# Performance work log

Measured on AMD Instinct MI355X. Metric: run time of the kernel, lower is better.

The kernel has to match this reference:

```python
import jax, jax.numpy as jnp
import numpy as np
import jax.ops

N_NODES = 50000
N_EDGES = 800000
N_GRAPHS = 512
F_IN = 128
HID = 256
N_CLASSES = 1

def _xavier(key, shape):
    fan_in, fan_out = shape[0], shape[1]
    std = (2.0 / (fan_in + fan_out)) ** 0.5
    return jax.random.normal(key, shape, dtype=jnp.float32) * std

def setup_inputs() -> dict:
    key = jax.random.key(0)
    ks = jax.random.split(key, 12)
    x = jax.random.normal(ks[0], (N_NODES, F_IN), dtype=jnp.float32)
    edge_index = jax.random.randint(ks[1], (2, N_EDGES), 0, N_NODES, dtype=jnp.int64)
    batch = jnp.sort(jax.random.randint(ks[2], (N_NODES,), 0, N_GRAPHS, dtype=jnp.int64))
    return {
        'x': x, 'edge_index': edge_index, 'batch': batch,
        'W0': _xavier(ks[3], (F_IN, HID)), 'b0': jnp.zeros((HID,), jnp.float32),
        'W1': _xavier(ks[4], (HID, HID)), 'b1': jnp.zeros((HID,), jnp.float32),
        'W2': _xavier(ks[5], (HID, HID)), 'b2': jnp.zeros((HID,), jnp.float32),
        'Wm1': _xavier(ks[6], (HID, HID)), 'bm1': jnp.zeros((HID,), jnp.float32),
        'Wm2': _xavier(ks[7], (HID, N_CLASSES)), 'bm2': jnp.zeros((N_CLASSES,), jnp.float32),
    }

def _gcn_layer(h, W, b, src, dst, deg_inv_sqrt):
    # PyG GCNConv: linear -> symmetric-normalized aggregation (with self loops) -> bias
    hw = h @ W                                        # [N, out]
    norm = deg_inv_sqrt[src] * deg_inv_sqrt[dst]      # [E]
    msg = hw[src] * norm[:, None]                     # [E, out]
    agg = jax.ops.segment_sum(msg, dst, num_segments=N_NODES)
    agg = agg + hw * (deg_inv_sqrt ** 2)[:, None]     # self-loop term
    return agg + b

def reference(x, edge_index, batch, W0, b0, W1, b1, W2, b2, Wm1, bm1, Wm2, bm2):
    src, dst = edge_index[0], edge_index[1]
    # degree with added self loops (in-degree at dst)
    deg = jax.ops.segment_sum(jnp.ones((N_EDGES,), jnp.float32), dst, num_segments=N_NODES) + 1.0
    deg_inv_sqrt = jax.lax.rsqrt(deg)
    h = jax.nn.relu(_gcn_layer(x, W0, b0, src, dst, deg_inv_sqrt))
    h = jax.nn.relu(_gcn_layer(h, W1, b1, src, dst, deg_inv_sqrt))
    h = jax.nn.relu(_gcn_layer(h, W2, b2, src, dst, deg_inv_sqrt))
    # global mean pool over graphs
    sums = jax.ops.segment_sum(h, batch, num_segments=N_GRAPHS)
    cnts = jax.ops.segment_sum(jnp.ones((N_NODES,), jnp.float32), batch, num_segments=N_GRAPHS)
    pooled = sums / jnp.maximum(cnts, 1.0)[:, None]   # [G, HID]
    out = jax.nn.relu(pooled @ Wm1 + bm1) @ Wm2 + bm2 # [G, num_classes]
    return out
```

## Files before the change

### kernel.cpp

```cpp
#include <hip/hip_runtime.h>

constexpr int N_NODES  = 50000;
constexpr int N_EDGES  = 800000;
constexpr int N_GRAPHS = 512;
constexpr int F_IN     = 128;
constexpr int HID      = 256;
constexpr int NPAD     = 50048;

typedef short short8 __attribute__((ext_vector_type(8)));
typedef float f32x4  __attribute__((ext_vector_type(4)));

__device__ __forceinline__ unsigned short f2b(float f) {
    unsigned u = __float_as_uint(f);
    u += 0x7fffu + ((u >> 16) & 1u);
    return (unsigned short)(u >> 16);
}
__device__ __forceinline__ float b2f_lo(unsigned u) { return __uint_as_float(u << 16); }
__device__ __forceinline__ float b2f_hi(unsigned u) { return __uint_as_float(u & 0xffff0000u); }

__global__ __launch_bounds__(256) void prep_kernel(
    const int* __restrict__ dst, int* __restrict__ deg,
    const float* __restrict__ x, unsigned short* __restrict__ x_bf,
    const float* __restrict__ W0, const float* __restrict__ W1, const float* __restrict__ W2,
    unsigned short* __restrict__ Wt0, unsigned short* __restrict__ Wt1, unsigned short* __restrict__ Wt2)
{
    const int b = blockIdx.x, t = threadIdx.x;
    if (b < 3125) {
        int e = b * 256 + t;
        atomicAdd(&deg[dst[e]], 1);
    } else if (b < 9375) {
        int i = (b - 3125) * 256 + t;
        float4 v = *reinterpret_cast<const float4*>(x + (size_t)i * 4);
        unsigned r0 = (unsigned)f2b(v.x) | ((unsigned)f2b(v.y) << 16);
        unsigned r1 = (unsigned)f2b(v.z) | ((unsigned)f2b(v.w) << 16);
        *reinterpret_cast<uint2*>(x_bf + (size_t)i * 4) = make_uint2(r0, r1);
    } else {
        int i = (b - 9375) * 256 + t;
        if (i < 32768)        { int k = i >> 8, n = i & 255;               Wt0[n * 128 + k] = f2b(W0[i]); }
        else if (i < 98304)   { int j = i - 32768; int k = j >> 8, n = j & 255; Wt1[n * 256 + k] = f2b(W1[j]); }
        else                  { int j = i - 98304; int k = j >> 8, n = j & 255; Wt2[n * 256 + k] = f2b(W2[j]); }
    }
}

__global__ void block_sum_dis_kernel(const int* __restrict__ deg, int* __restrict__ bsum,
                                     float* __restrict__ dis, int n) {
    __shared__ int sm[256];
    int t = threadIdx.x, base = blockIdx.x * 1024;
    int s = 0;
    #pragma unroll
    for (int i = 0; i < 4; ++i) {
        int idx = base + t + i * 256;
        if (idx < n) { int d = deg[idx]; s += d; dis[idx] = rsqrtf((float)d + 1.0f); }
    }
    sm[t] = s; __syncthreads();
    for (int o = 128; o > 0; o >>= 1) { if (t < o) sm[t] += sm[t + o]; __syncthreads(); }
    if (t == 0) bsum[blockIdx.x] = sm[0];
}

__global__ void scan_bsum_kernel(int* __restrict__ bsum, int nb) {
    __shared__ int sm[64];
    int t = threadIdx.x;
    int v = (t < nb) ? bsum[t] : 0;
    sm[t] = v; __syncthreads();
    for (int o = 1; o < 64; o <<= 1) {
        int a = (t >= o) ? sm[t - o] : 0; __syncthreads();
        sm[t] += a; __syncthreads();
    }
    if (t < nb) bsum[t] = sm[t] - v;
}

__global__ void scan_local_kernel(const int* __restrict__ deg, const int* __restrict__ bsum,
                                  int* __restrict__ row_start, int* __restrict__ cursor, int n) {
    __shared__ int sm[256];
    int t = threadIdx.x, base = blockIdx.x * 1024;
    int idx0 = base + t * 4;
    int v[4], s = 0;
    #pragma unroll
    for (int i = 0; i < 4; ++i) { int id = idx0 + i; v[i] = (id < n) ? deg[id] : 0; s += v[i]; }
    sm[t] = s; __syncthreads();
    for (int o = 1; o < 256; o <<= 1) {
        int a = (t >= o) ? sm[t - o] : 0; __syncthreads();
        sm[t] += a; __syncthreads();
    }
    int excl = bsum[blockIdx.x] + sm[t] - s;
    #pragma unroll
    for (int i = 0; i < 4; ++i) {
        int id = idx0 + i;
        if (id < n) { row_start[id] = excl; cursor[id] = excl; }
        excl += v[i];
    }
    if (blockIdx.x == gridDim.x - 1 && t == 255) row_start[n] = excl;
}

__global__ void fill_csr(const int* __restrict__ src, const int* __restrict__ dst,
                         const float* __restrict__ dis, int* __restrict__ cursor,
                         int2* __restrict__ csr) {
    int e = blockIdx.x * blockDim.x + threadIdx.x;
    if (e >= N_EDGES) return;
    int s = src[e], d = dst[e];
    int pos = atomicAdd(&cursor[d], 1);
    float w = dis[s] * dis[d];
    csr[pos] = make_int2(s, __float_as_int(w));
}

template<int F>
__global__ __launch_bounds__(256) void agg_bf16(
    const unsigned short* __restrict__ hin, const int* __restrict__ row_start,
    const int2* __restrict__ csr, const float* __restrict__ dis,
    unsigned short* __restrict__ out)
{
    constexpr int LPR  = F / 8;
    constexpr int NSUB = 64 / LPR;
    const int lane = threadIdx.x & 63;
    const int sub  = lane / LPR;
    const int fc   = lane % LPR;
    const int node = blockIdx.x * 4 + (threadIdx.x >> 6);
    if (node >= N_NODES) return;

    float acc[8];
    {
        float dn = dis[node];
        float sw = (sub == 0) ? dn * dn : 0.0f;
        uint2 u2[2];
        *reinterpret_cast<uint4*>(u2) =
            *reinterpret_cast<const uint4*>(hin + (size_t)node * F + fc * 8);
        #pragma unroll
        for (int h = 0; h < 2; ++h) {
            acc[h * 4 + 0] = b2f_lo(u2[h].x) * sw;
            acc[h * 4 + 1] = b2f_hi(u2[h].x) * sw;
            acc[h * 4 + 2] = b2f_lo(u2[h].y) * sw;
            acc[h * 4 + 3] = b2f_hi(u2[h].y) * sw;
        }
    }

    int j = row_start[node] + sub;
    const int end = row_start[node + 1];
    for (; j + 3 * NSUB < end; j += 4 * NSUB) {
        int2 c[4];
        #pragma unroll
        for (int u = 0; u < 4; ++u) c[u] = csr[j + u * NSUB];
        #pragma unroll
        for (int u = 0; u < 4; ++u) {
            float w = __int_as_float(c[u].y);
            uint2 g[2];
            *reinterpret_cast<uint4*>(g) =
                *reinterpret_cast<const uint4*>(hin + (size_t)c[u].x * F + fc * 8);
            #pragma unroll
            for (int h = 0; h < 2; ++h) {
                acc[h * 4 + 0] = fmaf(b2f_lo(g[h].x), w, acc[h * 4 + 0]);
                acc[h * 4 + 1] = fmaf(b2f_hi(g[h].x), w, acc[h * 4 + 1]);
                acc[h * 4 + 2] = fmaf(b2f_lo(g[h].y), w, acc[h * 4 + 2]);
                acc[h * 4 + 3] = fmaf(b2f_hi(g[h].y), w, acc[h * 4 + 3]);
            }
        }
    }
    for (; j < end; j += NSUB) {
        int2 c0 = csr[j];
        float w = __int_as_float(c0.y);
        uint2 g[2];
        *reinterpret_cast<uint4*>(g) =
            *reinterpret_cast<const uint4*>(hin + (size_t)c0.x * F + fc * 8);
        #pragma unroll
        for (int h = 0; h < 2; ++h) {
            acc[h * 4 + 0] = fmaf(b2f_lo(g[h].x), w, acc[h * 4 + 0]);
            acc[h * 4 + 1] = fmaf(b2f_hi(g[h].x), w, acc[h * 4 + 1]);
            acc[h * 4 + 2] = fmaf(b2f_lo(g[h].y), w, acc[h * 4 + 2]);
            acc[h * 4 + 3] = fmaf(b2f_hi(g[h].y), w, acc[h * 4 + 3]);
        }
    }

    #pragma unroll
    for (int k = 0; k < 8; ++k) {
        #pragma unroll
        for (int off = LPR; off < 64; off <<= 1)
            acc[k] += __shfl_xor(acc[k], off, 64);
    }

    if (sub == 0) {
        uint2 r[2];
        #pragma unroll
        for (int h = 0; h < 2; ++h) {
            r[h].x = (unsigned)f2b(acc[h * 4 + 0]) | ((unsigned)f2b(acc[h * 4 + 1]) << 16);
            r[h].y = (unsigned)f2b(acc[h * 4 + 2]) | ((unsigned)f2b(acc[h * 4 + 3]) << 16);
        }
        *reinterpret_cast<uint4*>(out + (size_t)node * F + fc * 8) =
            *reinterpret_cast<uint4*>(r);
    }
}

template<int K>
__global__ __launch_bounds__(256) void gemm_mfma(
    const unsigned short* __restrict__ A,
    const unsigned short* __restrict__ Bt,
    const float* __restrict__ bias,
    unsigned short* __restrict__ C,
    int relu)
{
    __shared__ __align__(16) unsigned short As[2][4 * 128 * 8];
    __shared__ __align__(16) unsigned short Bs[2][4 * 128 * 8];
    const int t    = threadIdx.x;
    const int lane = t & 63;
    const int w    = t >> 6;
    const int wm   = w & 1, wn = w >> 1;
    const int q    = lane >> 4, m = lane & 15;
    const int row0 = blockIdx.x * 128;
    const int col0 = blockIdx.y * 128;
    const int r_   = t >> 2, c_ = t & 3;

    f32x4 acc[4][4] = {};

    auto stage = [&](int buf, int k0) {
        #pragma unroll
        for (int pass = 0; pass < 2; ++pass) {
            int r = r_ + pass * 64;
            uint4 av = *reinterpret_cast<const uint4*>(A  + (size_t)(row0 + r) * K + k0 + c_ * 8);
            uint4 bv = *reinterpret_cast<const uint4*>(Bt + (size_t)(col0 + r) * K + k0 + c_ * 8);
            *reinterpret_cast<uint4*>(&As[buf][(c_ * 128 + r) * 8]) = av;
            *reinterpret_cast<uint4*>(&Bs[buf][(c_ * 128 + r) * 8]) = bv;
        }
    };

    constexpr int NK = K / 32;
    stage(0, 0);
    __syncthreads();
    #pragma unroll
    for (int kb = 0; kb < NK; ++kb) {
        if (kb + 1 < NK) stage((kb + 1) & 1, (kb + 1) * 32);
        const unsigned short* as = As[kb & 1];
        const unsigned short* bs = Bs[kb & 1];
        short8 af[4], bf[4];
        #pragma unroll
        for (int i = 0; i < 4; ++i)
            af[i] = *reinterpret_cast<const short8*>(&as[(q * 128 + wm * 64 + i * 16 + m) * 8]);
        #pragma unroll
        for (int jn = 0; jn < 4; ++jn)
            bf[jn] = *reinterpret_cast<const short8*>(&bs[(q * 128 + wn * 64 + jn * 16 + m) * 8]);
        #pragma unroll
        for (int i = 0; i < 4; ++i)
            #pragma unroll
            for (int jn = 0; jn < 4; ++jn)
                acc[i][jn] = __builtin_amdgcn_mfma_f32_16x16x32_bf16(af[i], bf[jn], acc[i][jn], 0, 0, 0);
        __syncthreads();
    }

    #pragma unroll
    for (int jn = 0; jn < 4; ++jn) {
        int col = col0 + wn * 64 + jn * 16 + m;
        float bj = bias[col];
        #pragma unroll
        for (int i = 0; i < 4; ++i) {
            int rowb = row0 + wm * 64 + i * 16 + q * 4;
            #pragma unroll
            for (int r = 0; r < 4; ++r) {
                float v = acc[i][jn][r] + bj;
                if (relu) v = fmaxf(v, 0.f);
                C[(size_t)(rowb + r) * 256 + col] = f2b(v);
            }
        }
    }
}

__global__ __launch_bounds__(256) void pool_mlp_kernel(
    const unsigned short* __restrict__ h, const int* __restrict__ batch,
    const float* __restrict__ Wm1, const float* __restrict__ bm1,
    const float* __restrict__ Wm2, const float* __restrict__ bm2,
    float* __restrict__ out)
{
    __shared__ float p[HID];
    __shared__ float red[HID];
    __shared__ int se[2];
    const int g = blockIdx.x, t = threadIdx.x;
    if (t < 2) {
        int target = g + t;
        int lo = 0, hi = N_NODES;
        while (lo < hi) { int mid = (lo + hi) >> 1; if (batch[mid] < target) lo = mid + 1; else hi = mid; }
        se[t] = lo;
    }
    __syncthreads();
    const int s = se[0], e = se[1];
    float acc = 0.f;
    for (int n = s; n < e; ++n) acc += b2f_lo((unsigned)h[(size_t)n * HID + t]);
    p[t] = acc / fmaxf((float)(e - s), 1.0f);
    __syncthreads();
    float a2 = bm1[t];
    for (int k = 0; k < HID; ++k) a2 = fmaf(p[k], Wm1[k * HID + t], a2);
    red[t] = fmaxf(a2, 0.f) * Wm2[t];
    __syncthreads();
    for (int o = 128; o > 0; o >>= 1) {
        if (t < o) red[t] += red[t + o];
        __syncthreads();
    }
    if (t == 0) out[g] = red[0] + bm2[0];
}

extern "C" void kernel_launch(void* const* d_in, const int* in_sizes, int n_in,
                              void* d_out, int out_size, void* d_ws, size_t ws_size,
                              hipStream_t stream) {
    const float* x    = (const float*)d_in[0];
    const int*   ei   = (const int*)d_in[1];
    const int*   batch= (const int*)d_in[2];
    const float* W0   = (const float*)d_in[3];
    const float* b0   = (const float*)d_in[4];
    const float* W1   = (const float*)d_in[5];
    const float* b1   = (const float*)d_in[6];
    const float* W2   = (const float*)d_in[7];
    const float* b2   = (const float*)d_in[8];
    const float* Wm1  = (const float*)d_in[9];
    const float* bm1  = (const float*)d_in[10];
    const float* Wm2  = (const float*)d_in[11];
    const float* bm2  = (const float*)d_in[12];
    float* out = (float*)d_out;

    char* ws = (char*)d_ws;
    size_t off = 0;
    auto alloc = [&](size_t bytes) -> void* {
        void* p = ws + off;
        off += (bytes + 255) & ~(size_t)255;
        return p;
    };
    int*   deg       = (int*)  alloc((size_t)N_NODES * 4);
    float* dis       = (float*)alloc((size_t)N_NODES * 4);
    int*   row_start = (int*)  alloc((size_t)(N_NODES + 1) * 4);
    int*   cursor    = (int*)  alloc((size_t)N_NODES * 4);
    int*   bsum      = (int*)  alloc((size_t)64 * 4);
    int2*  csr       = (int2*) alloc((size_t)N_EDGES * 8);
    unsigned short* x_bf = (unsigned short*)alloc((size_t)N_NODES * F_IN * 2);
    unsigned short* Wt0  = (unsigned short*)alloc((size_t)F_IN * HID * 2);
    unsigned short* Wt1  = (unsigned short*)alloc((size_t)HID * HID * 2);
    unsigned short* Wt2  = (unsigned short*)alloc((size_t)HID * HID * 2);
    unsigned short* bufA = (unsigned short*)alloc((size_t)NPAD * HID * 2);
    unsigned short* bufB = (unsigned short*)alloc((size_t)NPAD * HID * 2);

    const int* src = ei;
    const int* dst = ei + N_EDGES;
    const int NB = (N_NODES + 1023) / 1024;

    hipMemsetAsync(deg, 0, (size_t)N_NODES * 4, stream);
    prep_kernel        <<<10015, 256, 0, stream>>>(dst, deg, x, x_bf, W0, W1, W2, Wt0, Wt1, Wt2);
    block_sum_dis_kernel<<<NB, 256, 0, stream>>>(deg, bsum, dis, N_NODES);
    scan_bsum_kernel   <<<1, 64, 0, stream>>>(bsum, NB);
    scan_local_kernel  <<<NB, 256, 0, stream>>>(deg, bsum, row_start, cursor, N_NODES);
    fill_csr           <<<(N_EDGES + 255) / 256, 256, 0, stream>>>(src, dst, dis, cursor, csr);

    dim3 ggrid(NPAD / 128, 2);

    agg_bf16<F_IN><<<(N_NODES + 3) / 4, 256, 0, stream>>>(x_bf, row_start, csr, dis, bufA);
    gemm_mfma<F_IN><<<ggrid, 256, 0, stream>>>(bufA, Wt0, b0, bufB, 1);

    agg_bf16<HID><<<(N_NODES + 3) / 4, 256, 0, stream>>>(bufB, row_start, csr, dis, bufA);
    gemm_mfma<HID><<<ggrid, 256, 0, stream>>>(bufA, Wt1, b1, bufB, 1);

    agg_bf16<HID><<<(N_NODES + 3) / 4, 256, 0, stream>>>(bufB, row_start, csr, dis, bufA);
    gemm_mfma<HID><<<ggrid, 256, 0, stream>>>(bufA, Wt2, b2, bufB, 1);

    pool_mlp_kernel<<<N_GRAPHS, HID, 0, stream>>>(bufB, batch, Wm1, bm1, Wm2, bm2, out);
}
```

Before: 435.8 us.

## Write aggregation output in MFMA fragment layout and load A directly in GEMM

The aggregation kernel now writes its bf16 output in a panel/k-chunk-major layout that matches the MFMA A-fragment order. The GEMM reads A fragments straight from global memory without going through LDS, and the weights are pre-swizzled into fragment order and staged whole into LDS once per block. This removes the per-k-step A/B staging, the double buffering and the barriers. In exchange, A loads are no longer software-prefetched, and the LDS footprint is larger (64 KB for K=256), which may limit occupancy.

After: 430.9 us. About the same (-1.1%).

```diff
diff --git a/kernel.cpp b/kernel.cpp
--- a/kernel.cpp
+++ b/kernel.cpp
@@ -36,9 +36,13 @@
         *reinterpret_cast<uint2*>(x_bf + (size_t)i * 4) = make_uint2(r0, r1);
     } else {
         int i = (b - 9375) * 256 + t;
-        if (i < 32768)        { int k = i >> 8, n = i & 255;               Wt0[n * 128 + k] = f2b(W0[i]); }
-        else if (i < 98304)   { int j = i - 32768; int k = j >> 8, n = j & 255; Wt1[n * 256 + k] = f2b(W1[j]); }
-        else                  { int j = i - 98304; int k = j >> 8, n = j & 255; Wt2[n * 256 + k] = f2b(W2[j]); }
+        const float* W; unsigned short* Wt; int K; int j;
+        if (i < 32768)      { W = W0; Wt = Wt0; K = 128; j = i; }
+        else if (i < 98304) { W = W1; Wt = Wt1; K = 256; j = i - 32768; }
+        else                { W = W2; Wt = Wt2; K = 256; j = i - 98304; }
+        int k = j >> 8, n = j & 255;
+        int idx = (n >> 7) * (K * 128) + (((k >> 3) * 128 + (n & 127)) << 3) + (k & 7);
+        Wt[idx] = f2b(W[j]);
     }
 }
 
@@ -107,7 +111,7 @@
 __global__ __launch_bounds__(256) void agg_bf16(
     const unsigned short* __restrict__ hin, const int* __restrict__ row_start,
     const int2* __restrict__ csr, const float* __restrict__ dis,
-    unsigned short* __restrict__ out)
+    uint4* __restrict__ out4)
 {
     constexpr int LPR  = F / 8;
     constexpr int NSUB = 64 / LPR;
@@ -183,64 +187,56 @@
             r[h].x = (unsigned)f2b(acc[h * 4 + 0]) | ((unsigned)f2b(acc[h * 4 + 1]) << 16);
             r[h].y = (unsigned)f2b(acc[h * 4 + 2]) | ((unsigned)f2b(acc[h * 4 + 3]) << 16);
         }
-        *reinterpret_cast<uint4*>(out + (size_t)node * F + fc * 8) =
-            *reinterpret_cast<uint4*>(r);
+        int chunk = (node >> 7) * (128 * (F / 8)) + fc * 128 + (node & 127);
+        out4[chunk] = *reinterpret_cast<uint4*>(r);
     }
 }
 
 template<int K>
-__global__ __launch_bounds__(256) void gemm_mfma(
-    const unsigned short* __restrict__ A,
-    const unsigned short* __restrict__ Bt,
+__global__ __launch_bounds__(256) void gemm_frag(
+    const uint4* __restrict__ A4,
+    const unsigned short* __restrict__ Wt_frag,
     const float* __restrict__ bias,
     unsigned short* __restrict__ C,
     int relu)
 {
-    __shared__ __align__(16) unsigned short As[2][4 * 128 * 8];
-    __shared__ __align__(16) unsigned short Bs[2][4 * 128 * 8];
+    __shared__ __align__(16) unsigned short Bs[K * 128];
     const int t    = threadIdx.x;
     const int lane = t & 63;
     const int w    = t >> 6;
     const int wm   = w & 1, wn = w >> 1;
     const int q    = lane >> 4, m = lane & 15;
-    const int row0 = blockIdx.x * 128;
-    const int col0 = blockIdx.y * 128;
-    const int r_   = t >> 2, c_ = t & 3;
+    const int panel = blockIdx.x;
+    const int col0  = blockIdx.y * 128;
+
+    {
+        const uint4* src4 = reinterpret_cast<const uint4*>(Wt_frag + blockIdx.y * (K * 128));
+        uint4* dst4 = reinterpret_cast<uint4*>(Bs);
+        #pragma unroll
+        for (int it = 0; it < K / 16; ++it)
+            dst4[it * 256 + t] = src4[it * 256 + t];
+    }
+    __syncthreads();
 
     f32x4 acc[4][4] = {};
-
-    auto stage = [&](int buf, int k0) {
-        #pragma unroll
-        for (int pass = 0; pass < 2; ++pass) {
-            int r = r_ + pass * 64;
-            uint4 av = *reinterpret_cast<const uint4*>(A  + (size_t)(row0 + r) * K + k0 + c_ * 8);
-            uint4 bv = *reinterpret_cast<const uint4*>(Bt + (size_t)(col0 + r) * K + k0 + c_ * 8);
-            *reinterpret_cast<uint4*>(&As[buf][(c_ * 128 + r) * 8]) = av;
-            *reinterpret_cast<uint4*>(&Bs[buf][(c_ * 128 + r) * 8]) = bv;
-        }
-    };
-
-    constexpr int NK = K / 32;
-    stage(0, 0);
-    __syncthreads();
-    #pragma unroll
-    for (int kb = 0; kb < NK; ++kb) {
-        if (kb + 1 < NK) stage((kb + 1) & 1, (kb + 1) * 32);
-        const unsigned short* as = As[kb & 1];
-        const unsigned short* bs = Bs[kb & 1];
+    const int abase = panel * (128 * (K / 8));
+
+    #pragma unroll
+    for (int kb = 0; kb < K / 32; ++kb) {
         short8 af[4], bf[4];
         #pragma unroll
-        for (int i = 0; i < 4; ++i)
-            af[i] = *reinterpret_cast<const short8*>(&as[(q * 128 + wm * 64 + i * 16 + m) * 8]);
+        for (int i = 0; i < 4; ++i) {
+            uint4 v = A4[abase + (kb * 4 + q) * 128 + wm * 64 + i * 16 + m];
+            af[i] = *reinterpret_cast<short8*>(&v);
+        }
         #pragma unroll
         for (int jn = 0; jn < 4; ++jn)
-            bf[jn] = *reinterpret_cast<const short8*>(&bs[(q * 128 + wn * 64 + jn * 16 + m) * 8]);
+            bf[jn] = *reinterpret_cast<const short8*>(&Bs[((kb * 4 + q) * 128 + wn * 64 + jn * 16 + m) * 8]);
         #pragma unroll
         for (int i = 0; i < 4; ++i)
             #pragma unroll
             for (int jn = 0; jn < 4; ++jn)
                 acc[i][jn] = __builtin_amdgcn_mfma_f32_16x16x32_bf16(af[i], bf[jn], acc[i][jn], 0, 0, 0);
-        __syncthreads();
     }
 
     #pragma unroll
@@ -249,7 +245,7 @@
         float bj = bias[col];
         #pragma unroll
         for (int i = 0; i < 4; ++i) {
-            int rowb = row0 + wm * 64 + i * 16 + q * 4;
+            int rowb = panel * 128 + wm * 64 + i * 16 + q * 4;
             #pragma unroll
             for (int r = 0; r < 4; ++r) {
                 float v = acc[i][jn][r] + bj;
@@ -336,22 +332,22 @@
     const int NB = (N_NODES + 1023) / 1024;
 
     hipMemsetAsync(deg, 0, (size_t)N_NODES * 4, stream);
-    prep_kernel        <<<10015, 256, 0, stream>>>(dst, deg, x, x_bf, W0, W1, W2, Wt0, Wt1, Wt2);
+    prep_kernel         <<<10015, 256, 0, stream>>>(dst, deg, x, x_bf, W0, W1, W2, Wt0, Wt1, Wt2);
     block_sum_dis_kernel<<<NB, 256, 0, stream>>>(deg, bsum, dis, N_NODES);
-    scan_bsum_kernel   <<<1, 64, 0, stream>>>(bsum, NB);
-    scan_local_kernel  <<<NB, 256, 0, stream>>>(deg, bsum, row_start, cursor, N_NODES);
-    fill_csr           <<<(N_EDGES + 255) / 256, 256, 0, stream>>>(src, dst, dis, cursor, csr);
+    scan_bsum_kernel    <<<1, 64, 0, stream>>>(bsum, NB);
+    scan_local_kernel   <<<NB, 256, 0, stream>>>(deg, bsum, row_start, cursor, N_NODES);
+    fill_csr            <<<(N_EDGES + 255) / 256, 256, 0, stream>>>(src, dst, dis, cursor, csr);
 
     dim3 ggrid(NPAD / 128, 2);
 
-    agg_bf16<F_IN><<<(N_NODES + 3) / 4, 256, 0, stream>>>(x_bf, row_start, csr, dis, bufA);
-    gemm_mfma<F_IN><<<ggrid, 256, 0, stream>>>(bufA, Wt0, b0, bufB, 1);
-
-    agg_bf16<HID><<<(N_NODES + 3) / 4, 256, 0, stream>>>(bufB, row_start, csr, dis, bufA);
-    gemm_mfma<HID><<<ggrid, 256, 0, stream>>>(bufA, Wt1, b1, bufB, 1);
-
-    agg_bf16<HID><<<(N_NODES + 3) / 4, 256, 0, stream>>>(bufB, row_start, csr, dis, bufA);
-    gemm_mfma<HID><<<ggrid, 256, 0, stream>>>(bufA, Wt2, b2, bufB, 1);
+    agg_bf16<F_IN><<<(N_NODES + 3) / 4, 256, 0, stream>>>(x_bf, row_start, csr, dis, (uint4*)bufA);
+    gemm_frag<F_IN><<<ggrid, 256, 0, stream>>>((const uint4*)bufA, Wt0, b0, bufB, 1);
+
+    agg_bf16<HID><<<(N_NODES + 3) / 4, 256, 0, stream>>>(bufB, row_start, csr, dis, (uint4*)bufA);
+    gemm_frag<HID><<<ggrid, 256, 0, stream>>>((const uint4*)bufA, Wt1, b1, bufB, 1);
+
+    agg_bf16<HID><<<(N_NODES + 3) / 4, 256, 0, stream>>>(bufB, row_start, csr, dis, (uint4*)bufA);
+    gemm_frag<HID><<<ggrid, 256, 0, stream>>>((const uint4*)bufA, Wt2, b2, bufB, 1);
 
     pool_mlp_kernel<<<N_GRAPHS, HID, 0, stream>>>(bufB, batch, Wm1, bm1, Wm2, bm2, out);
 }
```

## Slice aggregation by feature chunk per XCD and pack CSR entries to 32 bits

Applied to the files above, without the earlier changes.

Aggregation now splits the feature dimension into 64-column slices and maps each slice to a fixed XCD via blockIdx&7, so each XCD's L2 only caches one slice of the gathered feature matrix. Each block walks 64 nodes in a loop instead of one node per wavefront. CSR entries shrink from 8 bytes to 4 by packing a 16-bit source index with a bf16 edge weight, which halves index traffic but loses weight precision and relies on node ids fitting in 16 bits (50000 < 65536). Separate h1/h2 buffers are used so layers can ping-pong.

After: 499.8 us. +14.7%, slower.

```diff
diff --git a/kernel.cpp b/kernel.cpp
--- a/kernel.cpp
+++ b/kernel.cpp
@@ -36,9 +36,12 @@
         *reinterpret_cast<uint2*>(x_bf + (size_t)i * 4) = make_uint2(r0, r1);
     } else {
         int i = (b - 9375) * 256 + t;
-        if (i < 32768)        { int k = i >> 8, n = i & 255;               Wt0[n * 128 + k] = f2b(W0[i]); }
-        else if (i < 98304)   { int j = i - 32768; int k = j >> 8, n = j & 255; Wt1[n * 256 + k] = f2b(W1[j]); }
-        else                  { int j = i - 98304; int k = j >> 8, n = j & 255; Wt2[n * 256 + k] = f2b(W2[j]); }
+        const float* W; unsigned short* Wt; int K; int j;
+        if (i < 32768)      { W = W0; Wt = Wt0; K = 128; j = i; }
+        else if (i < 98304) { W = W1; Wt = Wt1; K = 256; j = i - 32768; }
+        else                { W = W2; Wt = Wt2; K = 256; j = i - 98304; }
+        int k = j >> 8, n = j & 255;
+        Wt[n * K + k] = f2b(W[j]);
     }
 }
 
@@ -94,97 +97,110 @@
 
 __global__ void fill_csr(const int* __restrict__ src, const int* __restrict__ dst,
                          const float* __restrict__ dis, int* __restrict__ cursor,
-                         int2* __restrict__ csr) {
+                         unsigned* __restrict__ csr) {
     int e = blockIdx.x * blockDim.x + threadIdx.x;
     if (e >= N_EDGES) return;
     int s = src[e], d = dst[e];
     int pos = atomicAdd(&cursor[d], 1);
     float w = dis[s] * dis[d];
-    csr[pos] = make_int2(s, __float_as_int(w));
-}
-
-template<int F>
-__global__ __launch_bounds__(256) void agg_bf16(
+    csr[pos] = ((unsigned)f2b(w) << 16) | (unsigned)s;
+}
+
+template<int K, int NSLICE, int CHG>
+__global__ __launch_bounds__(256) void agg_sliced(
     const unsigned short* __restrict__ hin, const int* __restrict__ row_start,
-    const int2* __restrict__ csr, const float* __restrict__ dis,
+    const unsigned* __restrict__ csr, const float* __restrict__ dis,
     unsigned short* __restrict__ out)
 {
-    constexpr int LPR  = F / 8;
-    constexpr int NSUB = 64 / LPR;
-    const int lane = threadIdx.x & 63;
-    const int sub  = lane / LPR;
-    const int fc   = lane % LPR;
-    const int node = blockIdx.x * 4 + (threadIdx.x >> 6);
-    if (node >= N_NODES) return;
-
-    float acc[8];
-    {
-        float dn = dis[node];
-        float sw = (sub == 0) ? dn * dn : 0.0f;
-        uint2 u2[2];
-        *reinterpret_cast<uint4*>(u2) =
-            *reinterpret_cast<const uint4*>(hin + (size_t)node * F + fc * 8);
-        #pragma unroll
-        for (int h = 0; h < 2; ++h) {
-            acc[h * 4 + 0] = b2f_lo(u2[h].x) * sw;
-            acc[h * 4 + 1] = b2f_hi(u2[h].x) * sw;
-            acc[h * 4 + 2] = b2f_lo(u2[h].y) * sw;
-            acc[h * 4 + 3] = b2f_hi(u2[h].y) * sw;
-        }
-    }
-
-    int j = row_start[node] + sub;
-    const int end = row_start[node + 1];
-    for (; j + 3 * NSUB < end; j += 4 * NSUB) {
-        int2 c[4];
-        #pragma unroll
-        for (int u = 0; u < 4; ++u) c[u] = csr[j + u * NSUB];
-        #pragma unroll
-        for (int u = 0; u < 4; ++u) {
-            float w = __int_as_float(c[u].y);
-            uint2 g[2];
-            *reinterpret_cast<uint4*>(g) =
-                *reinterpret_cast<const uint4*>(hin + (size_t)c[u].x * F + fc * 8);
-            #pragma unroll
-            for (int h = 0; h < 2; ++h) {
-                acc[h * 4 + 0] = fmaf(b2f_lo(g[h].x), w, acc[h * 4 + 0]);
-                acc[h * 4 + 1] = fmaf(b2f_hi(g[h].x), w, acc[h * 4 + 1]);
-                acc[h * 4 + 2] = fmaf(b2f_lo(g[h].y), w, acc[h * 4 + 2]);
-                acc[h * 4 + 3] = fmaf(b2f_hi(g[h].y), w, acc[h * 4 + 3]);
-            }
-        }
-    }
-    for (; j < end; j += NSUB) {
-        int2 c0 = csr[j];
-        float w = __int_as_float(c0.y);
-        uint2 g[2];
-        *reinterpret_cast<uint4*>(g) =
-            *reinterpret_cast<const uint4*>(hin + (size_t)c0.x * F + fc * 8);
-        #pragma unroll
-        for (int h = 0; h < 2; ++h) {
-            acc[h * 4 + 0] = fmaf(b2f_lo(g[h].x), w, acc[h * 4 + 0]);
-            acc[h * 4 + 1] = fmaf(b2f_hi(g[h].x), w, acc[h * 4 + 1]);
-            acc[h * 4 + 2] = fmaf(b2f_lo(g[h].y), w, acc[h * 4 + 2]);
-            acc[h * 4 + 3] = fmaf(b2f_hi(g[h].y), w, acc[h * 4 + 3]);
-        }
-    }
-
-    #pragma unroll
-    for (int k = 0; k < 8; ++k) {
-        #pragma unroll
-        for (int off = LPR; off < 64; off <<= 1)
-            acc[k] += __shfl_xor(acc[k], off, 64);
-    }
-
-    if (sub == 0) {
-        uint2 r[2];
-        #pragma unroll
-        for (int h = 0; h < 2; ++h) {
-            r[h].x = (unsigned)f2b(acc[h * 4 + 0]) | ((unsigned)f2b(acc[h * 4 + 1]) << 16);
-            r[h].y = (unsigned)f2b(acc[h * 4 + 2]) | ((unsigned)f2b(acc[h * 4 + 3]) << 16);
-        }
-        *reinterpret_cast<uint4*>(out + (size_t)node * F + fc * 8) =
-            *reinterpret_cast<uint4*>(r);
+    const int b     = blockIdx.x;
+    const int xcd   = b & 7;
+    const int gp    = b >> 3;
+    const int slice = xcd % NSLICE;
+    const int chunk = gp + (xcd / NSLICE) * CHG;
+    const int t     = threadIdx.x;
+    const int lane  = t & 63;
+    const int w     = t >> 6;
+    const int sub   = lane >> 3;
+    const int fc    = lane & 7;
+    const int foff  = slice * 64 + fc * 8;
+
+    for (int nn = 0; nn < 16; ++nn) {
+        const int node = chunk * 64 + w * 16 + nn;
+        if (node >= N_NODES) break;
+
+        float acc[8];
+        {
+            float dn = dis[node];
+            float sw = (sub == 0) ? dn * dn : 0.0f;
+            uint2 u2[2];
+            *reinterpret_cast<uint4*>(u2) =
+                *reinterpret_cast<const uint4*>(hin + (size_t)node * K + foff);
+            #pragma unroll
+            for (int h = 0; h < 2; ++h) {
+                acc[h * 4 + 0] = b2f_lo(u2[h].x) * sw;
+                acc[h * 4 + 1] = b2f_hi(u2[h].x) * sw;
+                acc[h * 4 + 2] = b2f_lo(u2[h].y) * sw;
+                acc[h * 4 + 3] = b2f_hi(u2[h].y) * sw;
+            }
+        }
+
+        int j = row_start[node] + sub;
+        const int end = row_start[node + 1];
+        for (; j + 8 < end; j += 16) {
+            unsigned c0 = csr[j], c1 = csr[j + 8];
+            float w0 = b2f_hi(c0), w1 = b2f_hi(c1);
+            uint2 g0[2], g1[2];
+            *reinterpret_cast<uint4*>(g0) =
+                *reinterpret_cast<const uint4*>(hin + (size_t)(c0 & 0xffffu) * K + foff);
+            *reinterpret_cast<uint4*>(g1) =
+                *reinterpret_cast<const uint4*>(hin + (size_t)(c1 & 0xffffu) * K + foff);
+            #pragma unroll
+            for (int h = 0; h < 2; ++h) {
+                acc[h * 4 + 0] = fmaf(b2f_lo(g0[h].x), w0, acc[h * 4 + 0]);
+                acc[h * 4 + 1] = fmaf(b2f_hi(g0[h].x), w0, acc[h * 4 + 1]);
+                acc[h * 4 + 2] = fmaf(b2f_lo(g0[h].y), w0, acc[h * 4 + 2]);
+                acc[h * 4 + 3] = fmaf(b2f_hi(g0[h].y), w0, acc[h * 4 + 3]);
+            }
+            #pragma unroll
+            for (int h = 0; h < 2; ++h) {
+                acc[h * 4 + 0] = fmaf(b2f_lo(g1[h].x), w1, acc[h * 4 + 0]);
+                acc[h * 4 + 1] = fmaf(b2f_hi(g1[h].x), w1, acc[h * 4 + 1]);
+                acc[h * 4 + 2] = fmaf(b2f_lo(g1[h].y), w1, acc[h * 4 + 2]);
+                acc[h * 4 + 3] = fmaf(b2f_hi(g1[h].y), w1, acc[h * 4 + 3]);
+            }
+        }
+        if (j < end) {
+            unsigned c0 = csr[j];
+            float w0 = b2f_hi(c0);
+            uint2 g0[2];
+            *reinterpret_cast<uint4*>(g0) =
+                *reinterpret_cast<const uint4*>(hin + (size_t)(c0 & 0xffffu) * K + foff);
+            #pragma unroll
+            for (int h = 0; h < 2; ++h) {
+                acc[h * 4 + 0] = fmaf(b2f_lo(g0[h].x), w0, acc[h * 4 + 0]);
+                acc[h * 4 + 1] = fmaf(b2f_hi(g0[h].x), w0, acc[h * 4 + 1]);
+                acc[h * 4 + 2] = fmaf(b2f_lo(g0[h].y), w0, acc[h * 4 + 2]);
+                acc[h * 4 + 3] = fmaf(b2f_hi(g0[h].y), w0, acc[h * 4 + 3]);
+            }
+        }
+
+        #pragma unroll
+        for (int k = 0; k < 8; ++k) {
+            #pragma unroll
+            for (int off = 8; off < 64; off <<= 1)
+                acc[k] += __shfl_xor(acc[k], off, 64);
+        }
+
+        if (sub == 0) {
+            uint2 rv[2];
+            #pragma unroll
+            for (int h = 0; h < 2; ++h) {
+                rv[h].x = (unsigned)f2b(acc[h * 4 + 0]) | ((unsigned)f2b(acc[h * 4 + 1]) << 16);
+                rv[h].y = (unsigned)f2b(acc[h * 4 + 2]) | ((unsigned)f2b(acc[h * 4 + 3]) << 16);
+            }
+            *reinterpret_cast<uint4*>(out + (size_t)node * K + foff) =
+                *reinterpret_cast<uint4*>(rv);
+        }
     }
 }
 
@@ -318,40 +334,41 @@
         off += (bytes + 255) & ~(size_t)255;
         return p;
     };
-    int*   deg       = (int*)  alloc((size_t)N_NODES * 4);
-    float* dis       = (float*)alloc((size_t)N_NODES * 4);
-    int*   row_start = (int*)  alloc((size_t)(N_NODES + 1) * 4);
-    int*   cursor    = (int*)  alloc((size_t)N_NODES * 4);
-    int*   bsum      = (int*)  alloc((size_t)64 * 4);
-    int2*  csr       = (int2*) alloc((size_t)N_EDGES * 8);
+    int*      deg       = (int*)     alloc((size_t)N_NODES * 4);
+    float*    dis       = (float*)   alloc((size_t)N_NODES * 4);
+    int*      row_start = (int*)     alloc((size_t)(N_NODES + 1) * 4);
+    int*      cursor    = (int*)     alloc((size_t)N_NODES * 4);
+    int*      bsum      = (int*)     alloc((size_t)64 * 4);
+    unsigned* csr       = (unsigned*)alloc((size_t)N_EDGES * 4);
     unsigned short* x_bf = (unsigned short*)alloc((size_t)N_NODES * F_IN * 2);
     unsigned short* Wt0  = (unsigned short*)alloc((size_t)F_IN * HID * 2);
     unsigned short* Wt1  = (unsigned short*)alloc((size_t)HID * HID * 2);
     unsigned short* Wt2  = (unsigned short*)alloc((size_t)HID * HID * 2);
     unsigned short* bufA = (unsigned short*)alloc((size_t)NPAD * HID * 2);
-    unsigned short* bufB = (unsigned short*)alloc((size_t)NPAD * HID * 2);
+    unsigned short* h1   = (unsigned short*)alloc((size_t)NPAD * HID * 2);
+    unsigned short* h2   = (unsigned short*)alloc((size_t)NPAD * HID * 2);
 
     const int* src = ei;
     const int* dst = ei + N_EDGES;
     const int NB = (N_NODES + 1023) / 1024;
 
     hipMemsetAsync(deg, 0, (size_t)N_NODES * 4, stream);
-    prep_kernel        <<<10015, 256, 0, stream>>>(dst, deg, x, x_bf, W0, W1, W2, Wt0, Wt1, Wt2);
+    prep_kernel         <<<10015, 256, 0, stream>>>(dst, deg, x, x_bf, W0, W1, W2, Wt0, Wt1, Wt2);
     block_sum_dis_kernel<<<NB, 256, 0, stream>>>(deg, bsum, dis, N_NODES);
-    scan_bsum_kernel   <<<1, 64, 0, stream>>>(bsum, NB);
-    scan_local_kernel  <<<NB, 256, 0, stream>>>(deg, bsum, row_start, cursor, N_NODES);
-    fill_csr           <<<(N_EDGES + 255) / 256, 256, 0, stream>>>(src, dst, dis, cursor, csr);
+    scan_bsum_kernel    <<<1, 64, 0, stream>>>(bsum, NB);
+    scan_local_kernel   <<<NB, 256, 0, stream>>>(deg, bsum, row_start, cursor, N_NODES);
+    fill_csr            <<<(N_EDGES + 255) / 256, 256, 0, stream>>>(src, dst, dis, cursor, csr);
 
     dim3 ggrid(NPAD / 128, 2);
 
-    agg_bf16<F_IN><<<(N_NODES + 3) / 4, 256, 0, stream>>>(x_bf, row_start, csr, dis, bufA);
-    gemm_mfma<F_IN><<<ggrid, 256, 0, stream>>>(bufA, Wt0, b0, bufB, 1);
-
-    agg_bf16<HID><<<(N_NODES + 3) / 4, 256, 0, stream>>>(bufB, row_start, csr, dis, bufA);
-    gemm_mfma<HID><<<ggrid, 256, 0, stream>>>(bufA, Wt1, b1, bufB, 1);
-
-    agg_bf16<HID><<<(N_NODES + 3) / 4, 256, 0, stream>>>(bufB, row_start, csr, dis, bufA);
-    gemm_mfma<HID><<<ggrid, 256, 0, stream>>>(bufA, Wt2, b2, bufB, 1);
-
-    pool_mlp_kernel<<<N_GRAPHS, HID, 0, stream>>>(bufB, batch, Wm1, bm1, Wm2, bm2, out);
-}
+    agg_sliced<128, 2, 196><<<1568, 256, 0, stream>>>(x_bf, row_start, csr, dis, bufA);
+    gemm_mfma<128><<<ggrid, 256, 0, stream>>>(bufA, Wt0, b0, h1, 1);
+
+    agg_sliced<256, 4, 391><<<3128, 256, 0, stream>>>(h1, row_start, csr, dis, bufA);
+    gemm_mfma<256><<<ggrid, 256, 0, stream>>>(bufA, Wt1, b1, h2, 1);
+
+    agg_sliced<256, 4, 391><<<3128, 256, 0, stream>>>(h2, row_start, csr, dis, bufA);
+    gemm_mfma<256><<<ggrid, 256, 0, stream>>>(bufA, Wt2, b2, h1, 1);
+
+    pool_mlp_kernel<<<N_GRAPHS, HID, 0, stream>>>(h1, batch, Wm1, bm1, Wm2, bm2, out);
+}
```

## Fuse graph preprocessing into one cooperative kernel and pack CSR entries

Applied to the files above, without the earlier changes.

Replaces the memset, prep, block-sum, scan and CSR-fill launches with one cooperative kernel. Its phases (degree counting, scan, CSR fill) are separated by grid-wide syncs. CSR entries shrink from 8 bytes to 4 by packing a 16-bit source index with a bf16 edge weight. This cuts launch overhead and CSR bandwidth in the three aggregation passes, at the cost of lower precision in the edge weights and a grid size fixed by cooperative-launch occupancy.

Result: slower. 685.9 us (+57.4%).

```diff
diff --git a/kernel.cpp b/kernel.cpp
--- a/kernel.cpp
+++ b/kernel.cpp
@@ -1,4 +1,7 @@
 #include <hip/hip_runtime.h>
+#include <hip/hip_cooperative_groups.h>
+
+namespace cg = cooperative_groups;
 
 constexpr int N_NODES  = 50000;
 constexpr int N_EDGES  = 800000;
@@ -6,6 +9,8 @@
 constexpr int F_IN     = 128;
 constexpr int HID      = 256;
 constexpr int NPAD     = 50048;
+constexpr int PBLK     = 512;
+constexpr int SPAN     = 98;
 
 typedef short short8 __attribute__((ext_vector_type(8)));
 typedef float f32x4  __attribute__((ext_vector_type(4)));
@@ -18,98 +23,94 @@
 __device__ __forceinline__ float b2f_lo(unsigned u) { return __uint_as_float(u << 16); }
 __device__ __forceinline__ float b2f_hi(unsigned u) { return __uint_as_float(u & 0xffff0000u); }
 
-__global__ __launch_bounds__(256) void prep_kernel(
-    const int* __restrict__ dst, int* __restrict__ deg,
-    const float* __restrict__ x, unsigned short* __restrict__ x_bf,
+__device__ __forceinline__ int lds_scan_incl(int* sm, int v) {
+    const int t = threadIdx.x;
+    sm[t] = v; __syncthreads();
+    #pragma unroll
+    for (int o = 1; o < 256; o <<= 1) {
+        int a = (t >= o) ? sm[t - o] : 0; __syncthreads();
+        sm[t] += a; __syncthreads();
+    }
+    return sm[t];
+}
+
+__global__ __launch_bounds__(256, 2) void prep_all(
+    const int* __restrict__ src, const int* __restrict__ dst,
+    const float* __restrict__ x,
     const float* __restrict__ W0, const float* __restrict__ W1, const float* __restrict__ W2,
-    unsigned short* __restrict__ Wt0, unsigned short* __restrict__ Wt1, unsigned short* __restrict__ Wt2)
+    int* deg, float* dis, int* row_start, int* cursor, int* bsum, unsigned* csr,
+    unsigned short* x_bf, unsigned short* Wt0, unsigned short* Wt1, unsigned short* Wt2)
 {
-    const int b = blockIdx.x, t = threadIdx.x;
-    if (b < 3125) {
-        int e = b * 256 + t;
-        atomicAdd(&deg[dst[e]], 1);
-    } else if (b < 9375) {
-        int i = (b - 3125) * 256 + t;
+    __shared__ int sm[256];
+    cg::grid_group grid = cg::this_grid();
+    const int t   = threadIdx.x;
+    const int b   = blockIdx.x;
+    const int gid = b * 256 + t;
+    const int gstride = PBLK * 256;
+
+    for (int i = gid; i < N_NODES; i += gstride) deg[i] = 0;
+    for (int i = gid; i < N_NODES * F_IN / 4; i += gstride) {
         float4 v = *reinterpret_cast<const float4*>(x + (size_t)i * 4);
         unsigned r0 = (unsigned)f2b(v.x) | ((unsigned)f2b(v.y) << 16);
         unsigned r1 = (unsigned)f2b(v.z) | ((unsigned)f2b(v.w) << 16);
         *reinterpret_cast<uint2*>(x_bf + (size_t)i * 4) = make_uint2(r0, r1);
-    } else {
-        int i = (b - 9375) * 256 + t;
-        if (i < 32768)        { int k = i >> 8, n = i & 255;               Wt0[n * 128 + k] = f2b(W0[i]); }
-        else if (i < 98304)   { int j = i - 32768; int k = j >> 8, n = j & 255; Wt1[n * 256 + k] = f2b(W1[j]); }
-        else                  { int j = i - 98304; int k = j >> 8, n = j & 255; Wt2[n * 256 + k] = f2b(W2[j]); }
-    }
-}
-
-__global__ void block_sum_dis_kernel(const int* __restrict__ deg, int* __restrict__ bsum,
-                                     float* __restrict__ dis, int n) {
-    __shared__ int sm[256];
-    int t = threadIdx.x, base = blockIdx.x * 1024;
-    int s = 0;
-    #pragma unroll
-    for (int i = 0; i < 4; ++i) {
-        int idx = base + t + i * 256;
-        if (idx < n) { int d = deg[idx]; s += d; dis[idx] = rsqrtf((float)d + 1.0f); }
-    }
-    sm[t] = s; __syncthreads();
-    for (int o = 128; o > 0; o >>= 1) { if (t < o) sm[t] += sm[t + o]; __syncthreads(); }
-    if (t == 0) bsum[blockIdx.x] = sm[0];
-}
-
-__global__ void scan_bsum_kernel(int* __restrict__ bsum, int nb) {
-    __shared__ int sm[64];
-    int t = threadIdx.x;
-    int v = (t < nb) ? bsum[t] : 0;
-    sm[t] = v; __syncthreads();
-    for (int o = 1; o < 64; o <<= 1) {
-        int a = (t >= o) ? sm[t - o] : 0; __syncthreads();
-        sm[t] += a; __syncthreads();
-    }
-    if (t < nb) bsum[t] = sm[t] - v;
-}
-
-__global__ void scan_local_kernel(const int* __restrict__ deg, const int* __restrict__ bsum,
-                                  int* __restrict__ row_start, int* __restrict__ cursor, int n) {
-    __shared__ int sm[256];
-    int t = threadIdx.x, base = blockIdx.x * 1024;
-    int idx0 = base + t * 4;
-    int v[4], s = 0;
-    #pragma unroll
-    for (int i = 0; i < 4; ++i) { int id = idx0 + i; v[i] = (id < n) ? deg[id] : 0; s += v[i]; }
-    sm[t] = s; __syncthreads();
-    for (int o = 1; o < 256; o <<= 1) {
-        int a = (t >= o) ? sm[t - o] : 0; __syncthreads();
-        sm[t] += a; __syncthreads();
-    }
-    int excl = bsum[blockIdx.x] + sm[t] - s;
-    #pragma unroll
-    for (int i = 0; i < 4; ++i) {
-        int id = idx0 + i;
-        if (id < n) { row_start[id] = excl; cursor[id] = excl; }
-        excl += v[i];
-    }
-    if (blockIdx.x == gridDim.x - 1 && t == 255) row_start[n] = excl;
-}
-
-__global__ void fill_csr(const int* __restrict__ src, const int* __restrict__ dst,
-                         const float* __restrict__ dis, int* __restrict__ cursor,
-                         int2* __restrict__ csr) {
-    int e = blockIdx.x * blockDim.x + threadIdx.x;
-    if (e >= N_EDGES) return;
-    int s = src[e], d = dst[e];
-    int pos = atomicAdd(&cursor[d], 1);
-    float w = dis[s] * dis[d];
-    csr[pos] = make_int2(s, __float_as_int(w));
-}
-
-template<int F>
+    }
+    for (int i = gid; i < 163840; i += gstride) {
+        const float* W; unsigned short* Wt; int K, j;
+        if (i < 32768)      { W = W0; Wt = Wt0; K = 128; j = i; }
+        else if (i < 98304) { W = W1; Wt = Wt1; K = 256; j = i - 32768; }
+        else                { W = W2; Wt = Wt2; K = 256; j = i - 98304; }
+        int k = j >> 8, n = j & 255;
+        Wt[n * K + k] = f2b(W[j]);
+    }
+    grid.sync();
+
+    for (int e = gid; e < N_EDGES; e += gstride) atomicAdd(&deg[dst[e]], 1);
+    grid.sync();
+
+    {
+        int node = b * SPAN + t;
+        int d = 0;
+        if (t < SPAN && node < N_NODES) { d = deg[node]; dis[node] = rsqrtf((float)d + 1.0f); }
+        sm[t] = d; __syncthreads();
+        #pragma unroll
+        for (int o = 128; o > 0; o >>= 1) { if (t < o) sm[t] += sm[t + o]; __syncthreads(); }
+        if (t == 0) bsum[b] = sm[0];
+    }
+    grid.sync();
+
+    {
+        int pv = bsum[2 * t] + bsum[2 * t + 1];
+        lds_scan_incl(sm, pv);
+        const int p = b >> 1;
+        int Pb = (p > 0) ? sm[p - 1] : 0;
+        if (b & 1) Pb += bsum[2 * p];
+        const int grand = sm[255];
+        __syncthreads();
+        int node = b * SPAN + t;
+        int v = (t < SPAN && node < N_NODES) ? deg[node] : 0;
+        int incl = lds_scan_incl(sm, v);
+        int excl = incl - v + Pb;
+        if (t < SPAN && node < N_NODES) { row_start[node] = excl; cursor[node] = excl; }
+        if (b == PBLK - 1 && t == 0) row_start[N_NODES] = grand;
+    }
+    grid.sync();
+
+    for (int e = gid; e < N_EDGES; e += gstride) {
+        int s = src[e], d = dst[e];
+        int pos = atomicAdd(&cursor[d], 1);
+        float w = dis[s] * dis[d];
+        csr[pos] = ((unsigned)f2b(w) << 16) | (unsigned)s;
+    }
+}
+
+template<int K>
 __global__ __launch_bounds__(256) void agg_bf16(
     const unsigned short* __restrict__ hin, const int* __restrict__ row_start,
-    const int2* __restrict__ csr, const float* __restrict__ dis,
+    const unsigned* __restrict__ csr, const float* __restrict__ dis,
     unsigned short* __restrict__ out)
 {
-    constexpr int LPR  = F / 8;
+    constexpr int LPR  = K / 8;
     constexpr int NSUB = 64 / LPR;
     const int lane = threadIdx.x & 63;
     const int sub  = lane / LPR;
@@ -123,7 +124,7 @@
         float sw = (sub == 0) ? dn * dn : 0.0f;
         uint2 u2[2];
         *reinterpret_cast<uint4*>(u2) =
-            *reinterpret_cast<const uint4*>(hin + (size_t)node * F + fc * 8);
+            *reinterpret_cast<const uint4*>(hin + (size_t)node * K + fc * 8);
         #pragma unroll
         for (int h = 0; h < 2; ++h) {
             acc[h * 4 + 0] = b2f_lo(u2[h].x) * sw;
@@ -136,15 +137,15 @@
     int j = row_start[node] + sub;
     const int end = row_start[node + 1];
     for (; j + 3 * NSUB < end; j += 4 * NSUB) {
-        int2 c[4];
+        unsigned c[4];
         #pragma unroll
         for (int u = 0; u < 4; ++u) c[u] = csr[j + u * NSUB];
         #pragma unroll
         for (int u = 0; u < 4; ++u) {
-            float w = __int_as_float(c[u].y);
+            float w = b2f_hi(c[u]);
             uint2 g[2];
             *reinterpret_cast<uint4*>(g) =
-                *reinterpret_cast<const uint4*>(hin + (size_t)c[u].x * F + fc * 8);
+                *reinterpret_cast<const uint4*>(hin + (size_t)(c[u] & 0xffffu) * K + fc * 8);
             #pragma unroll
             for (int h = 0; h < 2; ++h) {
                 acc[h * 4 + 0] = fmaf(b2f_lo(g[h].x), w, acc[h * 4 + 0]);
@@ -155,11 +156,11 @@
         }
     }
     for (; j < end; j += NSUB) {
-        int2 c0 = csr[j];
-        float w = __int_as_float(c0.y);
+        unsigned c0 = csr[j];
+        float w = b2f_hi(c0);
         uint2 g[2];
         *reinterpret_cast<uint4*>(g) =
-            *reinterpret_cast<const uint4*>(hin + (size_t)c0.x * F + fc * 8);
+            *reinterpret_cast<const uint4*>(hin + (size_t)(c0 & 0xffffu) * K + fc * 8);
         #pragma unroll
         for (int h = 0; h < 2; ++h) {
             acc[h * 4 + 0] = fmaf(b2f_lo(g[h].x), w, acc[h * 4 + 0]);
@@ -177,14 +178,14 @@
     }
 
     if (sub == 0) {
-        uint2 r[2];
+        uint2 rv[2];
         #pragma unroll
         for (int h = 0; h < 2; ++h) {
-            r[h].x = (unsigned)f2b(acc[h * 4 + 0]) | ((unsigned)f2b(acc[h * 4 + 1]) << 16);
-            r[h].y = (unsigned)f2b(acc[h * 4 + 2]) | ((unsigned)f2b(acc[h * 4 + 3]) << 16);
-        }
-        *reinterpret_cast<uint4*>(out + (size_t)node * F + fc * 8) =
-            *reinterpret_cast<uint4*>(r);
+            rv[h].x = (unsigned)f2b(acc[h * 4 + 0]) | ((unsigned)f2b(acc[h * 4 + 1]) << 16);
+            rv[h].y = (unsigned)f2b(acc[h * 4 + 2]) | ((unsigned)f2b(acc[h * 4 + 3]) << 16);
+        }
+        *reinterpret_cast<uint4*>(out + (size_t)node * K + fc * 8) =
+            *reinterpret_cast<uint4*>(rv);
     }
 }
 
@@ -318,40 +319,41 @@
         off += (bytes + 255) & ~(size_t)255;
         return p;
     };
-    int*   deg       = (int*)  alloc((size_t)N_NODES * 4);
-    float* dis       = (float*)alloc((size_t)N_NODES * 4);
-    int*   row_start = (int*)  alloc((size_t)(N_NODES + 1) * 4);
-    int*   cursor    = (int*)  alloc((size_t)N_NODES * 4);
-    int*   bsum      = (int*)  alloc((size_t)64 * 4);
-    int2*  csr       = (int2*) alloc((size_t)N_EDGES * 8);
+    int*      deg       = (int*)     alloc((size_t)N_NODES * 4);
+    float*    dis       = (float*)   alloc((size_t)N_NODES * 4);
+    int*      row_start = (int*)     alloc((size_t)(N_NODES + 1) * 4);
+    int*      cursor    = (int*)     alloc((size_t)N_NODES * 4);
+    int*      bsum      = (int*)     alloc((size_t)PBLK * 4);
+    unsigned* csr       = (unsigned*)alloc((size_t)N_EDGES * 4);
     unsigned short* x_bf = (unsigned short*)alloc((size_t)N_NODES * F_IN * 2);
     unsigned short* Wt0  = (unsigned short*)alloc((size_t)F_IN * HID * 2);
     unsigned short* Wt1  = (unsigned short*)alloc((size_t)HID * HID * 2);
     unsigned short* Wt2  = (unsigned short*)alloc((size_t)HID * HID * 2);
     unsigned short* bufA = (unsigned short*)alloc((size_t)NPAD * HID * 2);
-    unsigned short* bufB = (unsigned short*)alloc((size_t)NPAD * HID * 2);
-
-    const int* src = ei;
-    const int* dst = ei + N_EDGES;
-    const int NB = (N_NODES + 1023) / 1024;
-
-    hipMemsetAsync(deg, 0, (size_t)N_NODES * 4, stream);
-    prep_kernel        <<<10015, 256, 0, stream>>>(dst, deg, x, x_bf, W0, W1, W2, Wt0, Wt1, Wt2);
-    block_sum_dis_kernel<<<NB, 256, 0, stream>>>(deg, bsum, dis, N_NODES);
-    scan_bsum_kernel   <<<1, 64, 0, stream>>>(bsum, NB);
-    scan_local_kernel  <<<NB, 256, 0, stream>>>(deg, bsum, row_start, cursor, N_NODES);
-    fill_csr           <<<(N_EDGES + 255) / 256, 256, 0, stream>>>(src, dst, dis, cursor, csr);
+    unsigned short* h1   = (unsigned short*)alloc((size_t)NPAD * HID * 2);
+    unsigned short* h2   = (unsigned short*)alloc((size_t)NPAD * HID * 2);
+
+    const int* srcp = ei;
+    const int* dstp = ei + N_EDGES;
+
+    void* pargs[] = {
+        (void*)&srcp, (void*)&dstp, (void*)&x,
+        (void*)&W0, (void*)&W1, (void*)&W2,
+        (void*)&deg, (void*)&dis, (void*)&row_start, (void*)&cursor, (void*)&bsum, (void*)&csr,
+        (void*)&x_bf, (void*)&Wt0, (void*)&Wt1, (void*)&Wt2
+    };
+    hipLaunchCooperativeKernel((void*)prep_all, dim3(PBLK), dim3(256), pargs, 0, stream);
 
     dim3 ggrid(NPAD / 128, 2);
 
     agg_bf16<F_IN><<<(N_NODES + 3) / 4, 256, 0, stream>>>(x_bf, row_start, csr, dis, bufA);
-    gemm_mfma<F_IN><<<ggrid, 256, 0, stream>>>(bufA, Wt0, b0, bufB, 1);
-
-    agg_bf16<HID><<<(N_NODES + 3) / 4, 256, 0, stream>>>(bufB, row_start, csr, dis, bufA);
-    gemm_mfma<HID><<<ggrid, 256, 0, stream>>>(bufA, Wt1, b1, bufB, 1);
-
-    agg_bf16<HID><<<(N_NODES + 3) / 4, 256, 0, stream>>>(bufB, row_start, csr, dis, bufA);
-    gemm_mfma<HID><<<ggrid, 256, 0, stream>>>(bufA, Wt2, b2, bufB, 1);
-
-    pool_mlp_kernel<<<N_GRAPHS, HID, 0, stream>>>(bufB, batch, Wm1, bm1, Wm2, bm2, out);
-}
+    gemm_mfma<F_IN><<<ggrid, 256, 0, stream>>>(bufA, Wt0, b0, h1, 1);
+
+    agg_bf16<HID><<<(N_NODES + 3) / 4, 256, 0, stream>>>(h1, row_start, csr, dis, bufA);
+    gemm_mfma<HID><<<ggrid, 256, 0, stream>>>(bufA, Wt1, b1, h2, 1);
+
+    agg_bf16<HID><<<(N_NODES + 3) / 4, 256, 0, stream>>>(h2, row_start, csr, dis, bufA);
+    gemm_mfma<HID><<<ggrid, 256, 0, stream>>>(bufA, Wt2, b2, h1, 1);
+
+    pool_mlp_kernel<<<N_GRAPHS, 256, 0, stream>>>(h1, batch, Wm1, bm1, Wm2, bm2, out);
+}
```
